# Performance work log

Measured on AMD Instinct MI355X. Metric: run time of the kernel, lower is better.

## Reference

```python
import jax, jax.numpy as jnp
import numpy as np

K = 2      # kernelsize
S = 2      # stride
FM = 32    # featuremaps


def extract_patches(x, k, s):
    """Mimic tf.image.extract_patches VALID: depth ordered (ki, kj, c)."""
    B, H, W, C = x.shape
    oh = (H - k) // s + 1
    ow = (W - k) // s + 1
    # k*k strided slices, each [B, oh, ow, C]; stacked -> [B, oh, ow, kk, C]
    cols = [x[:, i:i + s * oh:s, j:j + s * ow:s, :]
            for i in range(k) for j in range(k)]
    p = jnp.stack(cols, axis=3)
    return p.reshape(B, oh, ow, k * k * C)  # depth layout (ki, kj, c)


def setup_inputs() -> dict:
    key = jax.random.key(0)
    kx, k1, k2 = jax.random.split(key, 3)
    B, H, W, C = 8, 64, 64, 16
    kk = K * K
    x = jax.random.normal(kx, (B, H, W, C), dtype=jnp.float32)
    # VarianceScaling(2.0, untruncated_normal): std = sqrt(2/fan_in)
    W1 = jax.random.normal(k1, (C, kk, FM), dtype=jnp.float32) * np.sqrt(2.0 / kk)
    W2 = jax.random.normal(k2, (C, kk * kk, FM), dtype=jnp.float32) * np.sqrt(2.0 / (kk * kk))
    return {"x": x, "W1": W1, "W2": W2}


def reference(x, W1, W2):
    B, H, W_, C = x.shape
    kk = K * K
    pv = extract_patches(x, K, S)                 # [B, oh, ow, kk*C]
    oh, ow = pv.shape[1], pv.shape[2]
    # Faithful to source: raw reshape (NOT transpose) of (kk*C) -> (C, kk),
    # reinterpreting the (ki,kj,c)-ordered depth as rows of length kk.
    p = pv.reshape(B, oh, ow, C, kk)
    # tf.linalg.matmul([C,kk], [C,kk,F]) broadcasts -> z1[c,a,f] = sum_m p[a,m] W1[c,m,f]
    z1 = jnp.einsum('bhwam,cmf->bhwcaf', p, W1)
    # second-order outer product per row: [C, kk, kk] -> [C, kk*kk]
    so = (p[..., :, None] * p[..., None, :]).reshape(B, oh, ow, C, kk * kk)
    z2 = jnp.einsum('bhwaq,cqf->bhwcaf', so, W2)
    # per-patch [C, C, F] flattened to C*C*F channels, matching the source reshape
    return (z1 + z2).reshape(B, oh, ow, C * C * FM)
```

## Files before the change

kernel.cpp:

```cpp
#include <hip/hip_runtime.h>


typedef float f4 __attribute__((ext_vector_type(4)));

#define LPB 4

__global__ __launch_bounds__(256, 3) void quad_kernel(
    const float* __restrict__ x,
    const float* __restrict__ W1,
    const float* __restrict__ W2,
    float* __restrict__ out)
{
    const int t     = threadIdx.x;
    const int f4off = (t & 7) * 4;
    const int s     = t >> 3;
    const int c     = s & 15;
    const int half  = s >> 4;

    f4 w1r[4];
    f4 w2r[16];
    {
        const float* W1p = W1 + c * 128 + f4off;
#pragma unroll
        for (int m = 0; m < 4; ++m)
            w1r[m] = *(const f4*)(W1p + m * 32);
        const float* W2p = W2 + c * 512 + f4off;
#pragma unroll
        for (int q = 0; q < 16; ++q)
            w2r[q] = *(const f4*)(W2p + q * 32);
    }

    const int loc0 = blockIdx.x * LPB;

    for (int i = 0; i < LPB; ++i) {
        const int loc = loc0 + i;
        const int b  = loc >> 10;
        const int hw = loc & 1023;
        const int h  = hw >> 5;
        const int w  = hw & 31;

        const float* src =
            x + (((b * 64 + 2 * h + half) * 64) + 2 * w) * 16;
        f4 pv[8];
#pragma unroll
        for (int j = 0; j < 8; ++j)
            pv[j] = *(const f4*)(src + j * 4);

        float* outp = out + (size_t)loc * 8192 + c * 512 + half * 256 + f4off;

#pragma unroll
        for (int j = 0; j < 8; ++j) {
            const f4 P = pv[j];

            f4 t0 = w1r[0];
            f4 t1 = w1r[1];
            f4 t2 = w1r[2];
            f4 t3 = w1r[3];
            t0 += P.x * w2r[0];
            t1 += P.x * w2r[4];
            t2 += P.x * w2r[8];
            t3 += P.x * w2r[12];
            t0 += P.y * w2r[1];
            t1 += P.y * w2r[5];
            t2 += P.y * w2r[9];
            t3 += P.y * w2r[13];
            t0 += P.z * w2r[2];
            t1 += P.z * w2r[6];
            t2 += P.z * w2r[10];
            t3 += P.z * w2r[14];
            t0 += P.w * w2r[3];
            t1 += P.w * w2r[7];
            t2 += P.w * w2r[11];
            t3 += P.w * w2r[15];

            f4 acc = P.x * t0;
            acc += P.y * t1;
            acc += P.z * t2;
            acc += P.w * t3;

            __builtin_nontemporal_store(acc, (f4*)(outp + j * 32));
        }
    }
}

extern "C" void kernel_launch(void* const* d_in, const int* in_sizes, int n_in,
                              void* d_out, int out_size, void* d_ws, size_t ws_size,
                              hipStream_t stream) {
    const float* x  = (const float*)d_in[0];
    const float* W1 = (const float*)d_in[1];
    const float* W2 = (const float*)d_in[2];
    float* out = (float*)d_out;

    const int n_loc = 8 * 32 * 32;
    dim3 grid(n_loc / LPB), block(256);
    quad_kernel<<<grid, block, 0, stream>>>(x, W1, W2, out);
}
```

Before: 282.4 us.

## Remap threads so each warp stores contiguous 1KB output rows per channel

Changes the thread mapping so each 64-lane wavefront covers a contiguous 256-float output segment (8 patch rows × 32 features) for one channel, looping over 4 channels per wave and reloading the W1/W2 slices per channel. Patch values for all 4 locations are preloaded up front. The aim is fully coalesced contiguous stores instead of strided 128-byte chunks. It also drops the nontemporal store hint and the occupancy hint in launch bounds, and adds repeated weight loads (served from cache) per channel.

```diff
diff --git a/kernel.cpp b/kernel.cpp
--- a/kernel.cpp
+++ b/kernel.cpp
@@ -5,80 +5,72 @@
 
 #define LPB 4
 
-__global__ __launch_bounds__(256, 3) void quad_kernel(
+__global__ __launch_bounds__(256) void quad_kernel(
     const float* __restrict__ x,
     const float* __restrict__ W1,
     const float* __restrict__ W2,
     float* __restrict__ out)
 {
     const int t     = threadIdx.x;
-    const int f4off = (t & 7) * 4;
-    const int s     = t >> 3;
-    const int c     = s & 15;
-    const int half  = s >> 4;
-
-    f4 w1r[4];
-    f4 w2r[16];
-    {
-        const float* W1p = W1 + c * 128 + f4off;
-#pragma unroll
-        for (int m = 0; m < 4; ++m)
-            w1r[m] = *(const f4*)(W1p + m * 32);
-        const float* W2p = W2 + c * 512 + f4off;
-#pragma unroll
-        for (int q = 0; q < 16; ++q)
-            w2r[q] = *(const f4*)(W2p + q * 32);
-    }
+    const int w     = t >> 6;
+    const int lane  = t & 63;
+    const int A     = lane >> 3;
+    const int f4off = (lane & 7) * 4;
 
     const int loc0 = blockIdx.x * LPB;
 
-    for (int i = 0; i < LPB; ++i) {
-        const int loc = loc0 + i;
+    f4 P0[LPB], P1[LPB];
+#pragma unroll
+    for (int li = 0; li < LPB; ++li) {
+        const int loc = loc0 + li;
         const int b  = loc >> 10;
         const int hw = loc & 1023;
         const int h  = hw >> 5;
-        const int w  = hw & 31;
+        const int ww = hw & 31;
+        const float* row0 = x + (((b * 64 + 2 * h) * 64) + 2 * ww) * 16;
+        P0[li] = *(const f4*)(row0 + A * 4);
+        P1[li] = *(const f4*)(row0 + 64 * 16 + A * 4);
+    }
 
-        const float* src =
-            x + (((b * 64 + 2 * h + half) * 64) + 2 * w) * 16;
-        f4 pv[8];
+    float* const outb = out + (size_t)loc0 * 8192 + lane * 4;
+
+#pragma unroll 1
+    for (int cidx = 0; cidx < 4; ++cidx) {
+        const int c = w * 4 + cidx;
+
+        const float* W1p = W1 + c * 128 + f4off;
+        const float* W2p = W2 + c * 512 + f4off;
+        f4 w1r[4], w2r[16];
 #pragma unroll
-        for (int j = 0; j < 8; ++j)
-            pv[j] = *(const f4*)(src + j * 4);
+        for (int q = 0; q < 4; ++q)  w1r[q] = *(const f4*)(W1p + q * 32);
+#pragma unroll
+        for (int q = 0; q < 16; ++q) w2r[q] = *(const f4*)(W2p + q * 32);
 
-        float* outp = out + (size_t)loc * 8192 + c * 512 + half * 256 + f4off;
+        float* const outc = outb + c * 512;
 
 #pragma unroll
-        for (int j = 0; j < 8; ++j) {
-            const f4 P = pv[j];
+        for (int li = 0; li < LPB; ++li) {
+#pragma unroll
+            for (int half = 0; half < 2; ++half) {
+                const f4 P = half ? P1[li] : P0[li];
 
-            f4 t0 = w1r[0];
-            f4 t1 = w1r[1];
-            f4 t2 = w1r[2];
-            f4 t3 = w1r[3];
-            t0 += P.x * w2r[0];
-            t1 += P.x * w2r[4];
-            t2 += P.x * w2r[8];
-            t3 += P.x * w2r[12];
-            t0 += P.y * w2r[1];
-            t1 += P.y * w2r[5];
-            t2 += P.y * w2r[9];
-            t3 += P.y * w2r[13];
-            t0 += P.z * w2r[2];
-            t1 += P.z * w2r[6];
-            t2 += P.z * w2r[10];
-            t3 += P.z * w2r[14];
-            t0 += P.w * w2r[3];
-            t1 += P.w * w2r[7];
-            t2 += P.w * w2r[11];
-            t3 += P.w * w2r[15];
+                f4 t0 = w1r[0], t1 = w1r[1], t2 = w1r[2], t3 = w1r[3];
+                t0 += P.x * w2r[0];  t1 += P.x * w2r[4];
+                t2 += P.x * w2r[8];  t3 += P.x * w2r[12];
+                t0 += P.y * w2r[1];  t1 += P.y * w2r[5];
+                t2 += P.y * w2r[9];  t3 += P.y * w2r[13];
+                t0 += P.z * w2r[2];  t1 += P.z * w2r[6];
+                t2 += P.z * w2r[10]; t3 += P.z * w2r[14];
+                t0 += P.w * w2r[3];  t1 += P.w * w2r[7];
+                t2 += P.w * w2r[11]; t3 += P.w * w2r[15];
 
-            f4 acc = P.x * t0;
-            acc += P.y * t1;
-            acc += P.z * t2;
-            acc += P.w * t3;
+                f4 acc = P.x * t0;
+                acc += P.y * t1;
+                acc += P.z * t2;
+                acc += P.w * t3;
 
-            __builtin_nontemporal_store(acc, (f4*)(outp + j * 32));
+                *(f4*)(outc + (size_t)li * 8192 + half * 256) = acc;
+            }
         }
     }
 }
```

Result: faster. 273.7 us (-3.1%).
